# Kernel tuning notes

Measured on AMD Instinct MI355X. Metric: run time of the kernel, lower is better.

## Reference

```python
import jax, jax.numpy as jnp
import numpy as np

EPS = 1e-5


def setup_inputs() -> dict:
    key = jax.random.key(0)
    ks = jax.random.split(key, 6)
    B, H, W, C = 4, 64, 64, 64
    x_in = jax.random.normal(ks[0], (B, H, W, C), dtype=jnp.float32)
    scale = 1.0 / np.sqrt(C)
    w1 = jax.random.normal(ks[1], (C, C), dtype=jnp.float32) * scale
    w2 = jax.random.normal(ks[2], (C, C), dtype=jnp.float32) * scale
    w3 = jax.random.normal(ks[3], (C, C), dtype=jnp.float32) * scale
    w4 = jax.random.normal(ks[4], (C, C), dtype=jnp.float32) * scale
    zeros = jnp.zeros((C,), dtype=jnp.float32)
    return {
        "x_in": x_in,
        "w1": w1, "w2": w2, "w3": w3, "w4": w4,
        "b1": zeros, "b2": zeros, "b3": zeros, "b4": zeros,
        "gamma": jnp.ones((C,), dtype=jnp.float32),
        "beta": zeros,
    }


def reference(x_in, w1, w2, w3, w4, b1, b2, b3, b4, gamma, beta):
    B, H, W, C = x_in.shape
    # BatchNorm over batch + spatial dims, per channel (training-mode batch stats)
    mean = jnp.mean(x_in, axis=(0, 1, 2))            # [C]
    var = jnp.var(x_in, axis=(0, 1, 2))              # [C]
    x = (x_in - mean) * jax.lax.rsqrt(var + EPS) * gamma + beta
    # QKV projections
    q = jnp.einsum('bhwc,cC->bhwC', x, w1) + b1
    k = jnp.einsum('bhwc,cC->bhwC', x, w2) + b2
    v = jnp.einsum('bhwc,cC->bhwC', x, w3) + b3
    # Full spatial attention: [B, H, W, H, W]
    sdpa = jnp.einsum('bhwc,bHWc->bhwHW', q, k) / jnp.sqrt(jnp.float32(C))
    sdpa = jax.nn.softmax(sdpa.reshape(B, H, W, H * W), axis=-1)
    sdpa = sdpa.reshape(B, H, W, H, W)
    x = jnp.einsum('bhwHW,bHWc->bhwc', sdpa, v)
    # Output projection + residual
    x = jnp.einsum('bhwc,cC->bhwC', x, w4) + b4
    return x + x_in
```

## Files before the change

kernel.cpp:

```cpp
#include <hip/hip_runtime.h>

typedef _Float16 f16;
typedef _Float16 half2 __attribute__((ext_vector_type(2)));
typedef _Float16 half8 __attribute__((ext_vector_type(8)));
typedef float f32x4 __attribute__((ext_vector_type(4)));
typedef float f32x16 __attribute__((ext_vector_type(16)));
typedef unsigned u32x4 __attribute__((ext_vector_type(4)));

#define LDW 72

__global__ __launch_bounds__(256) void k_bnstats(const float* __restrict__ x, float* __restrict__ sums){
    __shared__ float red[512];
    int t = threadIdx.x;
    int c = t & 63, rg = t >> 6;
    int rb = blockIdx.x * 64;
    float s = 0.f, s2 = 0.f;
    for(int r = rg; r < 64; r += 4){
        float v = x[(rb + r) * 64 + c];
        s += v; s2 += v * v;
    }
    red[t] = s; red[256 + t] = s2;
    __syncthreads();
    if(t < 64){
        float a = red[t] + red[t + 64] + red[t + 128] + red[t + 192];
        float b = red[256 + t] + red[256 + t + 64] + red[256 + t + 128] + red[256 + t + 192];
        atomicAdd(&sums[c], a);
        atomicAdd(&sums[64 + c], b);
    }
}

__global__ __launch_bounds__(256) void k_qkv(
    const float* __restrict__ x,
    const float* __restrict__ w1, const float* __restrict__ w2, const float* __restrict__ w3,
    const float* __restrict__ b1, const float* __restrict__ b2, const float* __restrict__ b3,
    const float* __restrict__ gamma, const float* __restrict__ beta,
    const float* __restrict__ sums,
    f16* __restrict__ Q, f16* __restrict__ Kx, f16* __restrict__ Vt){
    __shared__ f16 wT[3 * 64 * LDW];
    __shared__ float sc[64], sh[64], bb[3][64];
    int t = threadIdx.x;
    for(int i = t; i < 3 * 4096; i += 256){
        int j = i >> 12, e = i & 4095, k = e >> 6, n = e & 63;
        const float* wp = (j == 0) ? w1 : ((j == 1) ? w2 : w3);
        wT[j * 64 * LDW + n * LDW + k] = (f16)wp[e];
    }
    if(t < 64){
        float mean = sums[t] * (1.f / 16384.f);
        float var  = sums[64 + t] * (1.f / 16384.f) - mean * mean;
        float s = gamma[t] * rsqrtf(var + 1e-5f);
        sc[t] = s;
        sh[t] = beta[t] - mean * s;
        bb[0][t] = b1[t]; bb[1][t] = b2[t]; bb[2][t] = b3[t];
    }
    __syncthreads();
    int w = t >> 6, lane = t & 63, quad = lane >> 4, l15 = lane & 15;
    int rowb = blockIdx.x * 64 + w * 16;
    int arow = rowb + l15;
    half8 a[2];
    #pragma unroll
    for(int kc = 0; kc < 2; kc++){
        f32x4 x0 = *(const f32x4*)&x[arow * 64 + kc * 32 + quad * 8];
        f32x4 x1 = *(const f32x4*)&x[arow * 64 + kc * 32 + quad * 8 + 4];
        half8 h;
        #pragma unroll
        for(int j = 0; j < 8; j++){
            int c = kc * 32 + quad * 8 + j;
            float xv = (j < 4) ? x0[j & 3] : x1[j & 3];
            h[j] = (f16)(xv * sc[c] + sh[c]);
        }
        a[kc] = h;
    }
    const f32x4 vzero = {0.f, 0.f, 0.f, 0.f};
    f32x4 acc[3][4];
    #pragma unroll
    for(int m = 0; m < 3; m++){
        #pragma unroll
        for(int nt = 0; nt < 4; nt++){
            acc[m][nt] = vzero;
            #pragma unroll
            for(int kc = 0; kc < 2; kc++){
                half8 bfr = *(half8*)&wT[m * 64 * LDW + (nt * 16 + l15) * LDW + kc * 32 + quad * 8];
                acc[m][nt] = __builtin_amdgcn_mfma_f32_16x16x32_f16(a[kc], bfr, acc[m][nt], 0, 0, 0);
            }
        }
    }
    const float qs = 0.18033688011112043f;
    #pragma unroll
    for(int nt = 0; nt < 4; nt++){
        #pragma unroll
        for(int r = 0; r < 4; r++){
            int row = rowb + quad * 4 + r;
            int col = nt * 16 + l15;
            Q[row * 64 + col]  = (f16)((acc[0][nt][r] + bb[0][col]) * qs);
            Kx[row * 64 + col] = (f16)(acc[1][nt][r] + bb[1][col]);
            Vt[((row >> 12) * 64 + col) * 4096 + (row & 4095)] = (f16)(acc[2][nt][r] + bb[2][col]);
        }
    }
}

__global__ __launch_bounds__(256, 2) void k_attn(
    const f16* __restrict__ Q, const f16* __restrict__ Kx, const f16* __restrict__ Vt,
    f16* __restrict__ Oph, float* __restrict__ lw){
    __shared__ f16 KV[2][2 * 64 * LDW];
    __shared__ float lred[4][64];
    int t = threadIdx.x;
    int kq = blockIdx.x & 7, qg = blockIdx.x >> 3;
    int b = qg >> 4;
    int w = t >> 6, lane = t & 63, l31 = lane & 31, hi = lane >> 5;
    int qrow0 = qg * 256 + w * 64;

    half8 aq[2][4];
    #pragma unroll
    for(int qt = 0; qt < 2; qt++)
        #pragma unroll
        for(int dc = 0; dc < 4; dc++)
            aq[qt][dc] = *(const half8*)&Q[(qrow0 + qt * 32 + l31) * 64 + dc * 16 + hi * 8];

    const f16* gsrc[4];
    int loff[4], gstep[4];
    #pragma unroll
    for(int i = 0; i < 4; i++){
        int idx = t + i * 256;
        int rr = (idx >> 3) & 63, c8 = idx & 7, kt0 = kq * 8;
        if(idx < 512){
            loff[i] = rr * LDW + c8 * 8;
            gsrc[i] = &Kx[(b * 4096 + kt0 * 64 + rr) * 64 + c8 * 8];
            gstep[i] = 64 * 64;
        } else {
            loff[i] = 64 * LDW + rr * LDW + c8 * 8;
            gsrc[i] = &Vt[(b * 64 + rr) * 4096 + kt0 * 64 + c8 * 8];
            gstep[i] = 64;
        }
    }
    half8 pre[4];
    #pragma unroll
    for(int i = 0; i < 4; i++){ pre[i] = *(const half8*)gsrc[i]; gsrc[i] += gstep[i]; }
    #pragma unroll
    for(int i = 0; i < 4; i++) *(half8*)&KV[0][loff[i]] = pre[i];

    f32x16 o[2][2];
    #pragma unroll
    for(int qt = 0; qt < 2; qt++)
        #pragma unroll
        for(int dt = 0; dt < 2; dt++)
            #pragma unroll
            for(int r = 0; r < 16; r++) o[qt][dt][r] = 0.f;
    float lp[2] = {0.f, 0.f};

    __syncthreads();
    int cur = 0;
    for(int j = 0; j < 8; j++){
        if(j < 7){
            #pragma unroll
            for(int i = 0; i < 4; i++){ pre[i] = *(const half8*)gsrc[i]; gsrc[i] += gstep[i]; }
        }
        const f16* Kb = &KV[cur][0];
        const f16* Vb = &KV[cur][64 * LDW];
        #pragma unroll
        for(int kt = 0; kt < 2; kt++){
            half8 ak[4];
            #pragma unroll
            for(int dc = 0; dc < 4; dc++)
                ak[dc] = *(const half8*)&Kb[(kt * 32 + l31) * LDW + dc * 16 + hi * 8];
            half8 vb[2][2];
            #pragma unroll
            for(int kc = 0; kc < 2; kc++)
                #pragma unroll
                for(int dt = 0; dt < 2; dt++)
                    vb[kc][dt] = *(const half8*)&Vb[(dt * 32 + l31) * LDW + kt * 32 + kc * 16 + hi * 8];
            #pragma unroll
            for(int qt = 0; qt < 2; qt++){
                f32x16 s;
                #pragma unroll
                for(int r = 0; r < 16; r++) s[r] = 0.f;
                #pragma unroll
                for(int dc = 0; dc < 4; dc++)
                    s = __builtin_amdgcn_mfma_f32_32x32x16_f16(ak[dc], aq[qt][dc], s, 0, 0, 0);
                float pf[16], ls = 0.f;
                #pragma unroll
                for(int r = 0; r < 16; r++){
                    float p = __builtin_amdgcn_exp2f(fminf(s[r], 15.f));
                    pf[r] = p; ls += p;
                }
                lp[qt] += ls;
                unsigned wv[4][2];
                #pragma unroll
                for(int g = 0; g < 4; g++){
                    wv[g][0] = __builtin_bit_cast(unsigned, __builtin_amdgcn_cvt_pkrtz(pf[4*g+0], pf[4*g+1]));
                    wv[g][1] = __builtin_bit_cast(unsigned, __builtin_amdgcn_cvt_pkrtz(pf[4*g+2], pf[4*g+3]));
                }
                #pragma unroll
                for(int kc = 0; kc < 2; kc++){
                    unsigned x0 = wv[2*kc][0], y0 = wv[2*kc+1][0];
                    unsigned x1 = wv[2*kc][1], y1 = wv[2*kc+1][1];
                    asm("v_permlane32_swap_b32 %0, %1" : "+v"(x0), "+v"(y0));
                    asm("v_permlane32_swap_b32 %0, %1" : "+v"(x1), "+v"(y1));
                    u32x4 pw = {x0, x1, y0, y1};
                    half8 pa = __builtin_bit_cast(half8, pw);
                    #pragma unroll
                    for(int dt = 0; dt < 2; dt++)
                        o[qt][dt] = __builtin_amdgcn_mfma_f32_32x32x16_f16(pa, vb[kc][dt], o[qt][dt], 0, 0, 0);
                }
            }
        }
        if(j < 7){
            f16* wb = &KV[cur ^ 1][0];
            #pragma unroll
            for(int i = 0; i < 4; i++) *(half8*)(wb + loff[i]) = pre[i];
        }
        cur ^= 1;
        __syncthreads();
    }
    #pragma unroll
    for(int qt = 0; qt < 2; qt++){
        float v = lp[qt] + __shfl_xor(lp[qt], 32);
        if(hi == 0){
            int row = qrow0 + qt * 32 + l31;
            lw[kq * 16384 + row] = v;
            lred[w][qt * 32 + l31] = __builtin_amdgcn_rcpf(v);
        }
    }
    #pragma unroll
    for(int qt = 0; qt < 2; qt++)
        #pragma unroll
        for(int r = 0; r < 16; r++){
            int qrl = qt * 32 + (r & 3) + 8 * (r >> 2) + 4 * hi;
            float inv = lred[w][qrl];
            int row = qrow0 + qrl;
            #pragma unroll
            for(int dt = 0; dt < 2; dt++)
                Oph[kq * 1048576 + row * 64 + dt * 32 + l31] = (f16)(o[qt][dt][r] * inv);
        }
}

__global__ __launch_bounds__(256) void k_merge(
    const f16* __restrict__ Oph, const float* __restrict__ lw,
    const float* __restrict__ w4, const float* __restrict__ b4,
    const float* __restrict__ x, float* __restrict__ out){
    __shared__ f16 Om[64 * LDW];
    __shared__ f16 wT[64 * LDW];
    __shared__ float b4f[64];
    int t = threadIdx.x;
    int rb = blockIdx.x * 64;
    for(int i = t; i < 4096; i += 256){
        int k = i >> 6, n = i & 63;
        wT[n * LDW + k] = (f16)w4[i];
    }
    if(t < 64) b4f[t] = b4[t];
    for(int i = t; i < 512; i += 256){
        int row = i >> 3, c8 = i & 7;
        int gr = rb + row;
        float num[8] = {0.f,0.f,0.f,0.f,0.f,0.f,0.f,0.f};
        float den = 0.f;
        #pragma unroll
        for(int s = 0; s < 8; s++){
            float li = lw[s * 16384 + gr];
            half8 ov = *(const half8*)&Oph[s * 1048576 + gr * 64 + c8 * 8];
            #pragma unroll
            for(int j = 0; j < 8; j++) num[j] += li * (float)ov[j];
            den += li;
        }
        float invd = 1.f / den;
        #pragma unroll
        for(int j = 0; j < 8; j++) Om[row * LDW + c8 * 8 + j] = (f16)(num[j] * invd);
    }
    __syncthreads();
    int w = t >> 6, lane = t & 63, quad = lane >> 4, l15 = lane & 15;
    half8 a[2];
    #pragma unroll
    for(int kc = 0; kc < 2; kc++)
        a[kc] = *(half8*)&Om[(w * 16 + l15) * LDW + kc * 32 + quad * 8];
    #pragma unroll
    for(int nt = 0; nt < 4; nt++){
        f32x4 y = {0.f, 0.f, 0.f, 0.f};
        #pragma unroll
        for(int kc = 0; kc < 2; kc++){
            half8 bfr = *(half8*)&wT[(nt * 16 + l15) * LDW + kc * 32 + quad * 8];
            y = __builtin_amdgcn_mfma_f32_16x16x32_f16(a[kc], bfr, y, 0, 0, 0);
        }
        #pragma unroll
        for(int r = 0; r < 4; r++){
            int row = rb + w * 16 + quad * 4 + r;
            int col = nt * 16 + l15;
            out[row * 64 + col] = y[r] + b4f[col] + x[row * 64 + col];
        }
    }
}

extern "C" void kernel_launch(void* const* d_in, const int* in_sizes, int n_in,
                              void* d_out, int out_size, void* d_ws, size_t ws_size,
                              hipStream_t stream){
    (void)in_sizes; (void)n_in; (void)out_size; (void)ws_size;
    const float* x  = (const float*)d_in[0];
    const float* w1 = (const float*)d_in[1];
    const float* w2 = (const float*)d_in[2];
    const float* w3 = (const float*)d_in[3];
    const float* w4 = (const float*)d_in[4];
    const float* b1 = (const float*)d_in[5];
    const float* b2 = (const float*)d_in[6];
    const float* b3 = (const float*)d_in[7];
    const float* b4 = (const float*)d_in[8];
    const float* gm = (const float*)d_in[9];
    const float* bt = (const float*)d_in[10];
    char* ws = (char*)d_ws;
    f16* Q   = (f16*)(ws);
    f16* Kx  = (f16*)(ws + (size_t)(2u << 20));
    f16* Vt  = (f16*)(ws + (size_t)(4u << 20));
    float* sums = (float*)(ws + (size_t)(6u << 20));
    f16* Oph = (f16*)(ws + (size_t)(6u << 20) + 1024);
    float* lwp = (float*)(ws + (size_t)(22u << 20) + 1024);

    hipMemsetAsync(sums, 0, 512, stream);
    hipLaunchKernelGGL(k_bnstats, dim3(256), dim3(256), 0, stream, x, sums);
    hipLaunchKernelGGL(k_qkv,     dim3(256), dim3(256), 0, stream, x, w1, w2, w3, b1, b2, b3, gm, bt, sums, Q, Kx, Vt);
    hipLaunchKernelGGL(k_attn,    dim3(512), dim3(256), 0, stream, Q, Kx, Vt, Oph, lwp);
    hipLaunchKernelGGL(k_merge,   dim3(256), dim3(256), 0, stream, Oph, lwp, w4, b4, x, (float*)d_out);
}
```

Measured before the change: 136.3 us.

## Fuse all stages into one cooperative kernel with grid-wide syncs

Replaces the memset plus four kernel launches with a single cooperative kernel of 256 blocks. Grid syncs separate the BN statistics, QKV projection, attention and merge/output-projection stages. This removes launch gaps and the memset. The cost is halving the attention grid: each block now processes two query groups serially instead of 512 blocks running at once. The original launches are kept as a fallback if the cooperative launch fails.

```diff
diff --git a/kernel.cpp b/kernel.cpp
--- a/kernel.cpp
+++ b/kernel.cpp
@@ -1,13 +1,309 @@
 #include <hip/hip_runtime.h>
+#include <hip/hip_cooperative_groups.h>
+
+namespace cg = cooperative_groups;
 
 typedef _Float16 f16;
-typedef _Float16 half2 __attribute__((ext_vector_type(2)));
 typedef _Float16 half8 __attribute__((ext_vector_type(8)));
 typedef float f32x4 __attribute__((ext_vector_type(4)));
 typedef float f32x16 __attribute__((ext_vector_type(16)));
 typedef unsigned u32x4 __attribute__((ext_vector_type(4)));
 
 #define LDW 72
+
+__global__ __launch_bounds__(256, 2) void k_fused(
+    const float* __restrict__ x,
+    const float* __restrict__ w1, const float* __restrict__ w2, const float* __restrict__ w3,
+    const float* __restrict__ w4,
+    const float* __restrict__ b1, const float* __restrict__ b2, const float* __restrict__ b3,
+    const float* __restrict__ b4,
+    const float* __restrict__ gamma, const float* __restrict__ beta,
+    float* __restrict__ sums,
+    f16* __restrict__ Q, f16* __restrict__ Kx, f16* __restrict__ Vt,
+    f16* __restrict__ Oph, float* __restrict__ lw,
+    float* __restrict__ out)
+{
+    __shared__ char smem[37888] __attribute__((aligned(16)));
+    cg::grid_group grid = cg::this_grid();
+    int t = threadIdx.x;
+    int bid = blockIdx.x;
+
+    {
+        f16*  wT  = (f16*)smem;
+        float* bb = (float*)(smem + 27648);
+        float* red = (float*)(smem + 28928);
+        for(int i = t; i < 3 * 4096; i += 256){
+            int j = i >> 12, e = i & 4095, k = e >> 6, n = e & 63;
+            const float* wp = (j == 0) ? w1 : ((j == 1) ? w2 : w3);
+            wT[j * 64 * LDW + n * LDW + k] = (f16)wp[e];
+        }
+        if(t < 64){ bb[t] = b1[t]; bb[64 + t] = b2[t]; bb[128 + t] = b3[t]; }
+        int c = t & 63, rg = t >> 6;
+        int rb = bid * 64;
+        float s = 0.f, s2 = 0.f;
+        for(int r = rg; r < 64; r += 4){
+            float v = x[(rb + r) * 64 + c];
+            s += v; s2 += v * v;
+        }
+        red[t] = s; red[256 + t] = s2;
+        if(bid == 0 && t < 128) sums[t] = 0.f;
+    }
+    grid.sync();
+    {
+        float* red = (float*)(smem + 28928);
+        if(t < 64){
+            float a = red[t] + red[t + 64] + red[t + 128] + red[t + 192];
+            float b = red[256 + t] + red[256 + t + 64] + red[256 + t + 128] + red[256 + t + 192];
+            atomicAdd(&sums[t], a);
+            atomicAdd(&sums[64 + t], b);
+        }
+    }
+    grid.sync();
+    {
+        f16*  wT  = (f16*)smem;
+        float* bb = (float*)(smem + 27648);
+        float* sc = (float*)(smem + 28416);
+        float* sh = (float*)(smem + 28672);
+        if(t < 64){
+            float mean = sums[t] * (1.f / 16384.f);
+            float var  = sums[64 + t] * (1.f / 16384.f) - mean * mean;
+            float s = gamma[t] * rsqrtf(var + 1e-5f);
+            sc[t] = s;
+            sh[t] = beta[t] - mean * s;
+        }
+        __syncthreads();
+        int w = t >> 6, lane = t & 63, quad = lane >> 4, l15 = lane & 15;
+        int rowb = bid * 64 + w * 16;
+        int arow = rowb + l15;
+        half8 a[2];
+        #pragma unroll
+        for(int kc = 0; kc < 2; kc++){
+            f32x4 x0 = *(const f32x4*)&x[arow * 64 + kc * 32 + quad * 8];
+            f32x4 x1 = *(const f32x4*)&x[arow * 64 + kc * 32 + quad * 8 + 4];
+            half8 h;
+            #pragma unroll
+            for(int j = 0; j < 8; j++){
+                int c = kc * 32 + quad * 8 + j;
+                float xv = (j < 4) ? x0[j & 3] : x1[j & 3];
+                h[j] = (f16)(xv * sc[c] + sh[c]);
+            }
+            a[kc] = h;
+        }
+        const f32x4 vzero = {0.f, 0.f, 0.f, 0.f};
+        f32x4 acc[3][4];
+        #pragma unroll
+        for(int m = 0; m < 3; m++){
+            #pragma unroll
+            for(int nt = 0; nt < 4; nt++){
+                acc[m][nt] = vzero;
+                #pragma unroll
+                for(int kc = 0; kc < 2; kc++){
+                    half8 bfr = *(half8*)&wT[m * 64 * LDW + (nt * 16 + l15) * LDW + kc * 32 + quad * 8];
+                    acc[m][nt] = __builtin_amdgcn_mfma_f32_16x16x32_f16(a[kc], bfr, acc[m][nt], 0, 0, 0);
+                }
+            }
+        }
+        const float qs = 0.18033688011112043f;
+        #pragma unroll
+        for(int nt = 0; nt < 4; nt++){
+            #pragma unroll
+            for(int r = 0; r < 4; r++){
+                int row = rowb + quad * 4 + r;
+                int col = nt * 16 + l15;
+                Q[row * 64 + col]  = (f16)((acc[0][nt][r] + bb[col]) * qs);
+                Kx[row * 64 + col] = (f16)(acc[1][nt][r] + bb[64 + col]);
+                Vt[((row >> 12) * 64 + col) * 4096 + (row & 4095)] = (f16)(acc[2][nt][r] + bb[128 + col]);
+            }
+        }
+    }
+    grid.sync();
+    {
+        f16* KV = (f16*)smem;
+        float* lred = (float*)(smem + 36864);
+        const int BUF = 2 * 64 * LDW;
+        int kq = bid & 7, qg = bid >> 3;
+        int w = t >> 6, lane = t & 63, l31 = lane & 31, hi = lane >> 5;
+
+        for(int half = 0; half < 2; half++){
+            int qg2 = qg * 2 + half;
+            int b = qg2 >> 4;
+            int qrow0 = qg2 * 256 + w * 64;
+
+            half8 aq[2][4];
+            #pragma unroll
+            for(int qt = 0; qt < 2; qt++)
+                #pragma unroll
+                for(int dc = 0; dc < 4; dc++)
+                    aq[qt][dc] = *(const half8*)&Q[(qrow0 + qt * 32 + l31) * 64 + dc * 16 + hi * 8];
+
+            const f16* gsrc[4];
+            int loff[4], gstep[4];
+            #pragma unroll
+            for(int i = 0; i < 4; i++){
+                int idx = t + i * 256;
+                int rr = (idx >> 3) & 63, c8 = idx & 7, kt0 = kq * 8;
+                if(idx < 512){
+                    loff[i] = rr * LDW + c8 * 8;
+                    gsrc[i] = &Kx[(b * 4096 + kt0 * 64 + rr) * 64 + c8 * 8];
+                    gstep[i] = 64 * 64;
+                } else {
+                    loff[i] = 64 * LDW + rr * LDW + c8 * 8;
+                    gsrc[i] = &Vt[(b * 64 + rr) * 4096 + kt0 * 64 + c8 * 8];
+                    gstep[i] = 64;
+                }
+            }
+            half8 pre[4];
+            #pragma unroll
+            for(int i = 0; i < 4; i++){ pre[i] = *(const half8*)gsrc[i]; gsrc[i] += gstep[i]; }
+            #pragma unroll
+            for(int i = 0; i < 4; i++) *(half8*)&KV[loff[i]] = pre[i];
+
+            f32x16 o[2][2];
+            #pragma unroll
+            for(int qt = 0; qt < 2; qt++)
+                #pragma unroll
+                for(int dt = 0; dt < 2; dt++)
+                    #pragma unroll
+                    for(int r = 0; r < 16; r++) o[qt][dt][r] = 0.f;
+            float lp[2] = {0.f, 0.f};
+
+            __syncthreads();
+            int cur = 0;
+            for(int j = 0; j < 8; j++){
+                if(j < 7){
+                    #pragma unroll
+                    for(int i = 0; i < 4; i++){ pre[i] = *(const half8*)gsrc[i]; gsrc[i] += gstep[i]; }
+                }
+                const f16* Kb = KV + cur * BUF;
+                const f16* Vb = Kb + 64 * LDW;
+                #pragma unroll
+                for(int kt = 0; kt < 2; kt++){
+                    half8 ak[4];
+                    #pragma unroll
+                    for(int dc = 0; dc < 4; dc++)
+                        ak[dc] = *(const half8*)&Kb[(kt * 32 + l31) * LDW + dc * 16 + hi * 8];
+                    half8 vb[2][2];
+                    #pragma unroll
+                    for(int kc = 0; kc < 2; kc++)
+                        #pragma unroll
+                        for(int dt = 0; dt < 2; dt++)
+                            vb[kc][dt] = *(const half8*)&Vb[(dt * 32 + l31) * LDW + kt * 32 + kc * 16 + hi * 8];
+                    #pragma unroll
+                    for(int qt = 0; qt < 2; qt++){
+                        f32x16 s;
+                        #pragma unroll
+                        for(int r = 0; r < 16; r++) s[r] = 0.f;
+                        #pragma unroll
+                        for(int dc = 0; dc < 4; dc++)
+                            s = __builtin_amdgcn_mfma_f32_32x32x16_f16(ak[dc], aq[qt][dc], s, 0, 0, 0);
+                        float pf[16], ls = 0.f;
+                        #pragma unroll
+                        for(int r = 0; r < 16; r++){
+                            float p = __builtin_amdgcn_exp2f(fminf(s[r], 15.f));
+                            pf[r] = p; ls += p;
+                        }
+                        lp[qt] += ls;
+                        unsigned wv[4][2];
+                        #pragma unroll
+                        for(int g = 0; g < 4; g++){
+                            wv[g][0] = __builtin_bit_cast(unsigned, __builtin_amdgcn_cvt_pkrtz(pf[4*g+0], pf[4*g+1]));
+                            wv[g][1] = __builtin_bit_cast(unsigned, __builtin_amdgcn_cvt_pkrtz(pf[4*g+2], pf[4*g+3]));
+                        }
+                        #pragma unroll
+                        for(int kc = 0; kc < 2; kc++){
+                            unsigned x0 = wv[2*kc][0], y0 = wv[2*kc+1][0];
+                            unsigned x1 = wv[2*kc][1], y1 = wv[2*kc+1][1];
+                            asm("v_permlane32_swap_b32 %0, %1" : "+v"(x0), "+v"(y0));
+                            asm("v_permlane32_swap_b32 %0, %1" : "+v"(x1), "+v"(y1));
+                            u32x4 pw = {x0, x1, y0, y1};
+                            half8 pa = __builtin_bit_cast(half8, pw);
+                            #pragma unroll
+                            for(int dt = 0; dt < 2; dt++)
+                                o[qt][dt] = __builtin_amdgcn_mfma_f32_32x32x16_f16(pa, vb[kc][dt], o[qt][dt], 0, 0, 0);
+                        }
+                    }
+                }
+                if(j < 7){
+                    f16* wb = KV + (cur ^ 1) * BUF;
+                    #pragma unroll
+                    for(int i = 0; i < 4; i++) *(half8*)(wb + loff[i]) = pre[i];
+                }
+                cur ^= 1;
+                __syncthreads();
+            }
+            #pragma unroll
+            for(int qt = 0; qt < 2; qt++){
+                float v = lp[qt] + __shfl_xor(lp[qt], 32);
+                if(hi == 0){
+                    int row = qrow0 + qt * 32 + l31;
+                    lw[kq * 16384 + row] = v;
+                    lred[w * 64 + qt * 32 + l31] = __builtin_amdgcn_rcpf(v);
+                }
+            }
+            #pragma unroll
+            for(int qt = 0; qt < 2; qt++)
+                #pragma unroll
+                for(int r = 0; r < 16; r++){
+                    int qrl = qt * 32 + (r & 3) + 8 * (r >> 2) + 4 * hi;
+                    float inv = lred[w * 64 + qrl];
+                    int row = qrow0 + qrl;
+                    #pragma unroll
+                    for(int dt = 0; dt < 2; dt++)
+                        Oph[kq * 1048576 + row * 64 + dt * 32 + l31] = (f16)(o[qt][dt][r] * inv);
+                }
+        }
+    }
+    grid.sync();
+    {
+        f16* Om  = (f16*)smem;
+        f16* wT4 = (f16*)(smem + 9216);
+        float* b4f = (float*)(smem + 18432);
+        int rb = bid * 64;
+        for(int i = t; i < 4096; i += 256){
+            int k = i >> 6, n = i & 63;
+            wT4[n * LDW + k] = (f16)w4[i];
+        }
+        if(t < 64) b4f[t] = b4[t];
+        for(int i = t; i < 512; i += 256){
+            int row = i >> 3, c8 = i & 7;
+            int gr = rb + row;
+            float num[8] = {0.f,0.f,0.f,0.f,0.f,0.f,0.f,0.f};
+            float den = 0.f;
+            #pragma unroll
+            for(int s = 0; s < 8; s++){
+                float li = lw[s * 16384 + gr];
+                half8 ov = *(const half8*)&Oph[s * 1048576 + gr * 64 + c8 * 8];
+                #pragma unroll
+                for(int j = 0; j < 8; j++) num[j] += li * (float)ov[j];
+                den += li;
+            }
+            float invd = 1.f / den;
+            #pragma unroll
+            for(int j = 0; j < 8; j++) Om[row * LDW + c8 * 8 + j] = (f16)(num[j] * invd);
+        }
+        __syncthreads();
+        int w = t >> 6, lane = t & 63, quad = lane >> 4, l15 = lane & 15;
+        half8 a[2];
+        #pragma unroll
+        for(int kc = 0; kc < 2; kc++)
+            a[kc] = *(half8*)&Om[(w * 16 + l15) * LDW + kc * 32 + quad * 8];
+        #pragma unroll
+        for(int nt = 0; nt < 4; nt++){
+            f32x4 y = {0.f, 0.f, 0.f, 0.f};
+            #pragma unroll
+            for(int kc = 0; kc < 2; kc++){
+                half8 bfr = *(half8*)&wT4[(nt * 16 + l15) * LDW + kc * 32 + quad * 8];
+                y = __builtin_amdgcn_mfma_f32_16x16x32_f16(a[kc], bfr, y, 0, 0, 0);
+            }
+            #pragma unroll
+            for(int r = 0; r < 4; r++){
+                int row = rb + w * 16 + quad * 4 + r;
+                int col = nt * 16 + l15;
+                out[row * 64 + col] = y[r] + b4f[col] + x[row * 64 + col];
+            }
+        }
+    }
+}
 
 __global__ __launch_bounds__(256) void k_bnstats(const float* __restrict__ x, float* __restrict__ sums){
     __shared__ float red[512];
@@ -108,6 +404,7 @@
     int b = qg >> 4;
     int w = t >> 6, lane = t & 63, l31 = lane & 31, hi = lane >> 5;
     int qrow0 = qg * 256 + w * 64;
+    const int BUF = 2 * 64 * LDW;
 
     half8 aq[2][4];
     #pragma unroll
@@ -154,8 +451,8 @@
             #pragma unroll
             for(int i = 0; i < 4; i++){ pre[i] = *(const half8*)gsrc[i]; gsrc[i] += gstep[i]; }
         }
-        const f16* Kb = &KV[cur][0];
-        const f16* Vb = &KV[cur][64 * LDW];
+        const f16* Kb = &KV[0][0] + cur * BUF;
+        const f16* Vb = Kb + 64 * LDW;
         #pragma unroll
         for(int kt = 0; kt < 2; kt++){
             half8 ak[4];
@@ -204,7 +501,7 @@
             }
         }
         if(j < 7){
-            f16* wb = &KV[cur ^ 1][0];
+            f16* wb = &KV[0][0] + (cur ^ 1) * BUF;
             #pragma unroll
             for(int i = 0; i < 4; i++) *(half8*)(wb + loff[i]) = pre[i];
         }
@@ -309,10 +606,22 @@
     float* sums = (float*)(ws + (size_t)(6u << 20));
     f16* Oph = (f16*)(ws + (size_t)(6u << 20) + 1024);
     float* lwp = (float*)(ws + (size_t)(22u << 20) + 1024);
-
-    hipMemsetAsync(sums, 0, 512, stream);
-    hipLaunchKernelGGL(k_bnstats, dim3(256), dim3(256), 0, stream, x, sums);
-    hipLaunchKernelGGL(k_qkv,     dim3(256), dim3(256), 0, stream, x, w1, w2, w3, b1, b2, b3, gm, bt, sums, Q, Kx, Vt);
-    hipLaunchKernelGGL(k_attn,    dim3(512), dim3(256), 0, stream, Q, Kx, Vt, Oph, lwp);
-    hipLaunchKernelGGL(k_merge,   dim3(256), dim3(256), 0, stream, Oph, lwp, w4, b4, x, (float*)d_out);
+    float* outp = (float*)d_out;
+
+    void* args[18];
+    args[0]  = (void*)&x;   args[1]  = (void*)&w1;  args[2]  = (void*)&w2;
+    args[3]  = (void*)&w3;  args[4]  = (void*)&w4;  args[5]  = (void*)&b1;
+    args[6]  = (void*)&b2;  args[7]  = (void*)&b3;  args[8]  = (void*)&b4;
+    args[9]  = (void*)&gm;  args[10] = (void*)&bt;  args[11] = (void*)&sums;
+    args[12] = (void*)&Q;   args[13] = (void*)&Kx;  args[14] = (void*)&Vt;
+    args[15] = (void*)&Oph; args[16] = (void*)&lwp; args[17] = (void*)&outp;
+
+    hipError_t rc = hipLaunchCooperativeKernel((const void*)k_fused, dim3(256), dim3(256), args, 0, stream);
+    if(rc != hipSuccess){
+        hipMemsetAsync(sums, 0, 512, stream);
+        hipLaunchKernelGGL(k_bnstats, dim3(256), dim3(256), 0, stream, x, sums);
+        hipLaunchKernelGGL(k_qkv,     dim3(256), dim3(256), 0, stream, x, w1, w2, w3, b1, b2, b3, gm, bt, sums, Q, Kx, Vt);
+        hipLaunchKernelGGL(k_attn,    dim3(512), dim3(256), 0, stream, Q, Kx, Vt, Oph, lwp);
+        hipLaunchKernelGGL(k_merge,   dim3(256), dim3(256), 0, stream, Oph, lwp, w4, b4, x, (float*)d_out);
+    }
 }
```

Result: slower. 251.0 us (+84.2%).

## Halve attention query tile per block and replace BN atomics with partial sums

Applied to the files above, without the earlier changes.

The attention kernel now handles 32 query rows per wave instead of 64, doubling the grid to 1024 blocks and raising the launch-bounds occupancy hint from 2 to 4 blocks per CU. Fewer accumulators per wave lower register pressure and should improve latency hiding. The cost is that K/V tiles are loaded from global memory twice as often per query. Separately, the BN statistics no longer use a memset plus atomics: each block writes per-channel partial sums, and k_qkv reduces the 256 partials itself, trading one small launch and atomic contention for a serial reduction in every qkv block.

```diff
diff --git a/kernel.cpp b/kernel.cpp
--- a/kernel.cpp
+++ b/kernel.cpp
@@ -1,7 +1,6 @@
 #include <hip/hip_runtime.h>
 
 typedef _Float16 f16;
-typedef _Float16 half2 __attribute__((ext_vector_type(2)));
 typedef _Float16 half8 __attribute__((ext_vector_type(8)));
 typedef float f32x4 __attribute__((ext_vector_type(4)));
 typedef float f32x16 __attribute__((ext_vector_type(16)));
@@ -9,7 +8,7 @@
 
 #define LDW 72
 
-__global__ __launch_bounds__(256) void k_bnstats(const float* __restrict__ x, float* __restrict__ sums){
+__global__ __launch_bounds__(256) void k_bnstats(const float* __restrict__ x, float* __restrict__ part){
     __shared__ float red[512];
     int t = threadIdx.x;
     int c = t & 63, rg = t >> 6;
@@ -21,11 +20,10 @@
     }
     red[t] = s; red[256 + t] = s2;
     __syncthreads();
-    if(t < 64){
-        float a = red[t] + red[t + 64] + red[t + 128] + red[t + 192];
-        float b = red[256 + t] + red[256 + t + 64] + red[256 + t + 128] + red[256 + t + 192];
-        atomicAdd(&sums[c], a);
-        atomicAdd(&sums[64 + c], b);
+    if(t < 128){
+        int c2 = t & 63, h = t >> 6;
+        float a = red[h * 256 + c2] + red[h * 256 + c2 + 64] + red[h * 256 + c2 + 128] + red[h * 256 + c2 + 192];
+        part[blockIdx.x * 128 + t] = a;
     }
 }
 
@@ -34,19 +32,29 @@
     const float* __restrict__ w1, const float* __restrict__ w2, const float* __restrict__ w3,
     const float* __restrict__ b1, const float* __restrict__ b2, const float* __restrict__ b3,
     const float* __restrict__ gamma, const float* __restrict__ beta,
-    const float* __restrict__ sums,
+    const float* __restrict__ part,
     f16* __restrict__ Q, f16* __restrict__ Kx, f16* __restrict__ Vt){
     __shared__ f16 wT[3 * 64 * LDW];
     __shared__ float sc[64], sh[64], bb[3][64];
+    __shared__ float psum[128];
     int t = threadIdx.x;
     for(int i = t; i < 3 * 4096; i += 256){
         int j = i >> 12, e = i & 4095, k = e >> 6, n = e & 63;
         const float* wp = (j == 0) ? w1 : ((j == 1) ? w2 : w3);
         wT[j * 64 * LDW + n * LDW + k] = (f16)wp[e];
     }
+    if(t < 128){
+        float a0 = 0.f, a1 = 0.f, a2 = 0.f, a3 = 0.f;
+        for(int b = 0; b < 256; b += 4){
+            a0 += part[b * 128 + t];       a1 += part[(b + 1) * 128 + t];
+            a2 += part[(b + 2) * 128 + t]; a3 += part[(b + 3) * 128 + t];
+        }
+        psum[t] = (a0 + a1) + (a2 + a3);
+    }
+    __syncthreads();
     if(t < 64){
-        float mean = sums[t] * (1.f / 16384.f);
-        float var  = sums[64 + t] * (1.f / 16384.f) - mean * mean;
+        float mean = psum[t] * (1.f / 16384.f);
+        float var  = psum[64 + t] * (1.f / 16384.f) - mean * mean;
         float s = gamma[t] * rsqrtf(var + 1e-5f);
         sc[t] = s;
         sh[t] = beta[t] - mean * s;
@@ -98,23 +106,22 @@
     }
 }
 
-__global__ __launch_bounds__(256, 2) void k_attn(
+__global__ __launch_bounds__(256, 4) void k_attn(
     const f16* __restrict__ Q, const f16* __restrict__ Kx, const f16* __restrict__ Vt,
     f16* __restrict__ Oph, float* __restrict__ lw){
     __shared__ f16 KV[2][2 * 64 * LDW];
-    __shared__ float lred[4][64];
+    __shared__ float lred[4][32];
     int t = threadIdx.x;
     int kq = blockIdx.x & 7, qg = blockIdx.x >> 3;
-    int b = qg >> 4;
+    int b = qg >> 5;
     int w = t >> 6, lane = t & 63, l31 = lane & 31, hi = lane >> 5;
-    int qrow0 = qg * 256 + w * 64;
-
-    half8 aq[2][4];
-    #pragma unroll
-    for(int qt = 0; qt < 2; qt++)
-        #pragma unroll
-        for(int dc = 0; dc < 4; dc++)
-            aq[qt][dc] = *(const half8*)&Q[(qrow0 + qt * 32 + l31) * 64 + dc * 16 + hi * 8];
+    int qrow0 = qg * 128 + w * 32;
+    const int BUF = 2 * 64 * LDW;
+
+    half8 aq[4];
+    #pragma unroll
+    for(int dc = 0; dc < 4; dc++)
+        aq[dc] = *(const half8*)&Q[(qrow0 + l31) * 64 + dc * 16 + hi * 8];
 
     const f16* gsrc[4];
     int loff[4], gstep[4];
@@ -138,14 +145,12 @@
     #pragma unroll
     for(int i = 0; i < 4; i++) *(half8*)&KV[0][loff[i]] = pre[i];
 
-    f32x16 o[2][2];
-    #pragma unroll
-    for(int qt = 0; qt < 2; qt++)
-        #pragma unroll
-        for(int dt = 0; dt < 2; dt++)
-            #pragma unroll
-            for(int r = 0; r < 16; r++) o[qt][dt][r] = 0.f;
-    float lp[2] = {0.f, 0.f};
+    f32x16 o[2];
+    #pragma unroll
+    for(int dt = 0; dt < 2; dt++)
+        #pragma unroll
+        for(int r = 0; r < 16; r++) o[dt][r] = 0.f;
+    float lp = 0.f;
 
     __syncthreads();
     int cur = 0;
@@ -154,8 +159,8 @@
             #pragma unroll
             for(int i = 0; i < 4; i++){ pre[i] = *(const half8*)gsrc[i]; gsrc[i] += gstep[i]; }
         }
-        const f16* Kb = &KV[cur][0];
-        const f16* Vb = &KV[cur][64 * LDW];
+        const f16* Kb = &KV[0][0] + cur * BUF;
+        const f16* Vb = Kb + 64 * LDW;
         #pragma unroll
         for(int kt = 0; kt < 2; kt++){
             half8 ak[4];
@@ -168,69 +173,63 @@
                 #pragma unroll
                 for(int dt = 0; dt < 2; dt++)
                     vb[kc][dt] = *(const half8*)&Vb[(dt * 32 + l31) * LDW + kt * 32 + kc * 16 + hi * 8];
-            #pragma unroll
-            for(int qt = 0; qt < 2; qt++){
-                f32x16 s;
+            f32x16 s;
+            #pragma unroll
+            for(int r = 0; r < 16; r++) s[r] = 0.f;
+            #pragma unroll
+            for(int dc = 0; dc < 4; dc++)
+                s = __builtin_amdgcn_mfma_f32_32x32x16_f16(ak[dc], aq[dc], s, 0, 0, 0);
+            float pf[16], ls = 0.f;
+            #pragma unroll
+            for(int r = 0; r < 16; r++){
+                float p = __builtin_amdgcn_exp2f(fminf(s[r], 15.f));
+                pf[r] = p; ls += p;
+            }
+            lp += ls;
+            unsigned wv[4][2];
+            #pragma unroll
+            for(int g = 0; g < 4; g++){
+                wv[g][0] = __builtin_bit_cast(unsigned, __builtin_amdgcn_cvt_pkrtz(pf[4*g+0], pf[4*g+1]));
+                wv[g][1] = __builtin_bit_cast(unsigned, __builtin_amdgcn_cvt_pkrtz(pf[4*g+2], pf[4*g+3]));
+            }
+            #pragma unroll
+            for(int kc = 0; kc < 2; kc++){
+                unsigned x0 = wv[2*kc][0], y0 = wv[2*kc+1][0];
+                unsigned x1 = wv[2*kc][1], y1 = wv[2*kc+1][1];
+                asm("v_permlane32_swap_b32 %0, %1" : "+v"(x0), "+v"(y0));
+                asm("v_permlane32_swap_b32 %0, %1" : "+v"(x1), "+v"(y1));
+                u32x4 pw = {x0, x1, y0, y1};
+                half8 pa = __builtin_bit_cast(half8, pw);
                 #pragma unroll
-                for(int r = 0; r < 16; r++) s[r] = 0.f;
-                #pragma unroll
-                for(int dc = 0; dc < 4; dc++)
-                    s = __builtin_amdgcn_mfma_f32_32x32x16_f16(ak[dc], aq[qt][dc], s, 0, 0, 0);
-                float pf[16], ls = 0.f;
-                #pragma unroll
-                for(int r = 0; r < 16; r++){
-                    float p = __builtin_amdgcn_exp2f(fminf(s[r], 15.f));
-                    pf[r] = p; ls += p;
-                }
-                lp[qt] += ls;
-                unsigned wv[4][2];
-                #pragma unroll
-                for(int g = 0; g < 4; g++){
-                    wv[g][0] = __builtin_bit_cast(unsigned, __builtin_amdgcn_cvt_pkrtz(pf[4*g+0], pf[4*g+1]));
-                    wv[g][1] = __builtin_bit_cast(unsigned, __builtin_amdgcn_cvt_pkrtz(pf[4*g+2], pf[4*g+3]));
-                }
-                #pragma unroll
-                for(int kc = 0; kc < 2; kc++){
-                    unsigned x0 = wv[2*kc][0], y0 = wv[2*kc+1][0];
-                    unsigned x1 = wv[2*kc][1], y1 = wv[2*kc+1][1];
-                    asm("v_permlane32_swap_b32 %0, %1" : "+v"(x0), "+v"(y0));
-                    asm("v_permlane32_swap_b32 %0, %1" : "+v"(x1), "+v"(y1));
-                    u32x4 pw = {x0, x1, y0, y1};
-                    half8 pa = __builtin_bit_cast(half8, pw);
-                    #pragma unroll
-                    for(int dt = 0; dt < 2; dt++)
-                        o[qt][dt] = __builtin_amdgcn_mfma_f32_32x32x16_f16(pa, vb[kc][dt], o[qt][dt], 0, 0, 0);
-                }
+                for(int dt = 0; dt < 2; dt++)
+                    o[dt] = __builtin_amdgcn_mfma_f32_32x32x16_f16(pa, vb[kc][dt], o[dt], 0, 0, 0);
             }
         }
         if(j < 7){
-            f16* wb = &KV[cur ^ 1][0];
+            f16* wb = &KV[0][0] + (cur ^ 1) * BUF;
             #pragma unroll
             for(int i = 0; i < 4; i++) *(half8*)(wb + loff[i]) = pre[i];
         }
         cur ^= 1;
         __syncthreads();
     }
-    #pragma unroll
-    for(int qt = 0; qt < 2; qt++){
-        float v = lp[qt] + __shfl_xor(lp[qt], 32);
+    {
+        float v = lp + __shfl_xor(lp, 32);
         if(hi == 0){
-            int row = qrow0 + qt * 32 + l31;
+            int row = qrow0 + l31;
             lw[kq * 16384 + row] = v;
-            lred[w][qt * 32 + l31] = __builtin_amdgcn_rcpf(v);
-        }
-    }
-    #pragma unroll
-    for(int qt = 0; qt < 2; qt++)
-        #pragma unroll
-        for(int r = 0; r < 16; r++){
-            int qrl = qt * 32 + (r & 3) + 8 * (r >> 2) + 4 * hi;
-            float inv = lred[w][qrl];
-            int row = qrow0 + qrl;
-            #pragma unroll
-            for(int dt = 0; dt < 2; dt++)
-                Oph[kq * 1048576 + row * 64 + dt * 32 + l31] = (f16)(o[qt][dt][r] * inv);
-        }
+            lred[w][l31] = __builtin_amdgcn_rcpf(v);
+        }
+    }
+    #pragma unroll
+    for(int r = 0; r < 16; r++){
+        int qrl = (r & 3) + 8 * (r >> 2) + 4 * hi;
+        float inv = lred[w][qrl];
+        int row = qrow0 + qrl;
+        #pragma unroll
+        for(int dt = 0; dt < 2; dt++)
+            Oph[kq * 1048576 + row * 64 + dt * 32 + l31] = (f16)(o[dt][r] * inv);
+    }
 }
 
 __global__ __launch_bounds__(256) void k_merge(
@@ -303,16 +302,15 @@
     const float* gm = (const float*)d_in[9];
     const float* bt = (const float*)d_in[10];
     char* ws = (char*)d_ws;
-    f16* Q   = (f16*)(ws);
-    f16* Kx  = (f16*)(ws + (size_t)(2u << 20));
-    f16* Vt  = (f16*)(ws + (size_t)(4u << 20));
-    float* sums = (float*)(ws + (size_t)(6u << 20));
-    f16* Oph = (f16*)(ws + (size_t)(6u << 20) + 1024);
-    float* lwp = (float*)(ws + (size_t)(22u << 20) + 1024);
-
-    hipMemsetAsync(sums, 0, 512, stream);
-    hipLaunchKernelGGL(k_bnstats, dim3(256), dim3(256), 0, stream, x, sums);
-    hipLaunchKernelGGL(k_qkv,     dim3(256), dim3(256), 0, stream, x, w1, w2, w3, b1, b2, b3, gm, bt, sums, Q, Kx, Vt);
-    hipLaunchKernelGGL(k_attn,    dim3(512), dim3(256), 0, stream, Q, Kx, Vt, Oph, lwp);
-    hipLaunchKernelGGL(k_merge,   dim3(256), dim3(256), 0, stream, Oph, lwp, w4, b4, x, (float*)d_out);
-}
+    f16* Q    = (f16*)(ws);
+    f16* Kx   = (f16*)(ws + (size_t)(2u << 20));
+    f16* Vt   = (f16*)(ws + (size_t)(4u << 20));
+    float* part = (float*)(ws + (size_t)(6u << 20));
+    f16* Oph  = (f16*)(ws + (size_t)(8u << 20));
+    float* lwp = (float*)(ws + (size_t)(24u << 20));
+
+    hipLaunchKernelGGL(k_bnstats, dim3(256),  dim3(256), 0, stream, x, part);
+    hipLaunchKernelGGL(k_qkv,     dim3(256),  dim3(256), 0, stream, x, w1, w2, w3, b1, b2, b3, gm, bt, part, Q, Kx, Vt);
+    hipLaunchKernelGGL(k_attn,    dim3(1024), dim3(256), 0, stream, Q, Kx, Vt, Oph, lwp);
+    hipLaunchKernelGGL(k_merge,   dim3(256),  dim3(256), 0, stream, Oph, lwp, w4, b4, x, (float*)d_out);
+}
```

Result: faster. 130.9 us (-4.0%).
